# Kernel tuning notes

Hardware: AMD Instinct MI355X
Metric: run time of the kernel (lower is better)

The kernel has to match this reference:

```python
import jax, jax.numpy as jnp
import numpy as np

B, D_DATA, D_DICT0, N_SAE, D_DICT = 2048, 768, 128, 128, 32


def _kaiming_uniform(key, shape, fan_in):
    # torch.nn.init.kaiming_uniform_ default: bound = sqrt(6 / fan_in) / sqrt(5-gain stuff) ~ use gain=sqrt(2)? match torch default a=sqrt(5) not needed; plain kaiming_uniform_ uses gain=sqrt(2): bound = sqrt(6/fan_in)*? Keep simple: bound = sqrt(6.0/fan_in)
    bound = np.sqrt(6.0 / fan_in)
    return jax.random.uniform(key, shape, jnp.float32, -bound, bound)


def setup_inputs() -> dict:
    key = jax.random.key(0)
    ks = jax.random.split(key, 6)
    x = jax.random.normal(ks[0], (B, D_DATA), jnp.float32)
    # top-level SAE params
    W_enc0 = _kaiming_uniform(ks[1], (D_DATA, D_DICT0), D_DATA)
    b_enc0 = jnp.zeros((D_DICT0,), jnp.float32)
    W_dec0 = _kaiming_uniform(ks[2], (D_DICT0, D_DATA), D_DICT0)
    W_dec0 = W_dec0 / jnp.linalg.norm(W_dec0, axis=-1, keepdims=True)
    b_dec0 = jnp.zeros((D_DATA,), jnp.float32)
    # sublayer (hierarchical) per-expert params
    W_enc1 = _kaiming_uniform(ks[3], (N_SAE, D_DATA, D_DICT), D_DATA)
    b_enc1 = jnp.zeros((N_SAE, D_DICT), jnp.float32)
    W_dec1 = _kaiming_uniform(ks[4], (N_SAE, D_DICT, D_DATA), D_DICT)
    W_dec1 = W_dec1 / jnp.linalg.norm(W_dec1, axis=-1, keepdims=True)
    b_dec1 = jnp.zeros((N_SAE, D_DATA), jnp.float32)
    return {"x": x, "W_enc0": W_enc0, "b_enc0": b_enc0, "W_dec0": W_dec0,
            "b_dec0": b_dec0, "W_enc1": W_enc1, "b_enc1": b_enc1,
            "W_dec1": W_dec1, "b_dec1": b_dec1}


def reference(x, W_enc0, b_enc0, W_dec0, b_dec0, W_enc1, b_enc1, W_dec1, b_dec1):
    # ---- sae_0 (standard SAE; scale/unscale are identity) ----
    acts0 = jax.nn.relu((x - b_dec0) @ W_enc0 + b_enc0)        # [B, D_DICT0]
    x0 = acts0 @ W_dec0 + b_dec0                               # [B, D_DATA]
    # ---- binary gate over experts (n_sae == d_dict0) ----
    gate = (acts0 > 0).astype(x.dtype)                         # [B, N_SAE]
    # ---- sublayer: gather-encode-decode-scatter, expressed densely with a
    # binary mask (gate only selects membership; gate value is not multiplied).
    # Avoid materializing [B, N_SAE, D_DATA] by distributing (x - b_dec1[j]):
    pre = (jnp.einsum('bd,jdk->bjk', x, W_enc1)
           - jnp.einsum('jd,jdk->jk', b_dec1, W_enc1)[None]
           + b_enc1[None])                                     # [B, N_SAE, D_DICT]
    acts1 = jax.nn.relu(pre) * gate[:, :, None]                # zero out ungated
    # scatter_add over experts: sum_j gated (acts1[b,j] @ W_dec1[j] + b_dec1[j])
    dec = jnp.einsum('bjk,jkd->bd', acts1, W_dec1) + gate @ b_dec1  # [B, D_DATA]
    return x0 + dec
```

## Files before the change

kernel.cpp:

```cpp
#include <hip/hip_runtime.h>
#include <hip/hip_bf16.h>
#include <stdint.h>

#define B_SZ   2048
#define DDATA  768
#define NSAE   128
#define NJK    4096
#define KA2    4352
#define SPLITK 2
#define KC2    2176
#define GZCH   8
#define GZW    96

typedef unsigned short u16;
typedef short bf16x8 __attribute__((ext_vector_type(8)));
typedef float f32x4  __attribute__((ext_vector_type(4)));

static __device__ __forceinline__ u16 f2bf(float f) {
  __hip_bfloat16 h = __float2bfloat16(f);
  return *reinterpret_cast<u16*>(&h);
}

static __device__ __forceinline__ void gload16(const u16* g, u16* l) {
  __builtin_amdgcn_global_load_lds(
      (const __attribute__((address_space(1))) unsigned int*)g,
      (__attribute__((address_space(3))) unsigned int*)l,
      16, 0, 0);
}

__global__ __launch_bounds__(256) void k_front(const float* __restrict__ x,
                                               const float* __restrict__ We0,
                                               const float* __restrict__ bd0,
                                               const float* __restrict__ We1,
                                               const float* __restrict__ bd1,
                                               const float* __restrict__ be1,
                                               const float* __restrict__ Wd1,
                                               const float* __restrict__ Wd0,
                                               u16* __restrict__ W1T,
                                               float* __restrict__ cv,
                                               u16* __restrict__ B2T,
                                               u16* __restrict__ xb,
                                               float* __restrict__ pp,
                                               float* __restrict__ xnp,
                                               float* __restrict__ wn) {
  __shared__ float smem[64 * 65];
  const int bid = blockIdx.x, t = threadIdx.x;
  if (bid < 128) {
    const int j = bid;
    float* ts  = smem;
    float* bds = smem + 64 * 33;
    float* red = smem + 64 * 33 + 64;
    const int k = t & 31, g = t >> 5;
    float cacc = 0.f;
    for (int db = 0; db < 12; ++db) {
      const float* src = We1 + (size_t)j * 24576 + db * 2048;
#pragma unroll
      for (int i = 0; i < 8; ++i) {
        int e = t + i * 256;
        ts[(e >> 5) * 33 + (e & 31)] = src[e];
      }
      if (t < 64) bds[t] = bd1[(size_t)j * DDATA + db * 64 + t];
      __syncthreads();
#pragma unroll
      for (int i = 0; i < 8; ++i) {
        int e = t + i * 256;
        int kk = e >> 6, d = e & 63;
        W1T[(size_t)(j * 32 + kk) * DDATA + db * 64 + d] = f2bf(ts[d * 33 + kk]);
      }
#pragma unroll
      for (int q = 0; q < 8; ++q) {
        int d = g + 8 * q;
        cacc += ts[d * 33 + k] * bds[d];
      }
      __syncthreads();
    }
    red[g * 32 + k] = cacc;
    __syncthreads();
    if (g == 0) {
      float s = 0.f;
#pragma unroll
      for (int q = 0; q < 8; ++q) s += red[q * 32 + k];
      cv[j * 32 + k] = be1[j * 32 + k] - s;
    }
  } else if (bid < 944) {
    const int e2 = bid - 128;
    const int rb = e2 / 12, dbk = e2 % 12;
    const float* src; int r0, base;
    if (rb < 64)      { src = Wd1; r0 = rb * 64;        base = 0;    }
    else if (rb < 66) { src = Wd0; r0 = (rb - 64) * 64; base = 4096; }
    else              { src = bd1; r0 = (rb - 66) * 64; base = 4224; }
    const int d0 = dbk * 64;
#pragma unroll
    for (int i = 0; i < 16; ++i) {
      int e = t + i * 256;
      int ri = e >> 6, di = e & 63;
      smem[ri * 65 + di] = src[(size_t)(r0 + ri) * DDATA + d0 + di];
    }
    __syncthreads();
#pragma unroll
    for (int i = 0; i < 16; ++i) {
      int e = t + i * 256;
      int di = e >> 6, ri = e & 63;
      B2T[(size_t)(d0 + di) * KA2 + base + r0 + ri] = f2bf(smem[ri * 65 + di]);
    }
  } else if (bid < 952) {
    const int wb = bid - 944;
    const int jj = wb * 16 + (t >> 4), s = t & 15;
    float acc = 0.f;
    for (int d = s; d < DDATA; d += 16) {
      float w = We0[(size_t)d * 128 + jj];
      acc += w * w;
    }
#pragma unroll
    for (int sh = 8; sh; sh >>= 1) acc += __shfl_xor(acc, sh, 64);
    if (s == 0) wn[jj] = sqrtf(acc);
  } else {
    const int bid2 = bid - 952;
    const int b0 = (bid2 & 63) * 32, z = bid2 >> 6;
    const int dbase = z * GZW;
    float* xs = smem;
#pragma unroll
    for (int i = 0; i < 3; ++i) {
      int idx = t + i * 256;
      int r = idx / 24, c4 = idx % 24;
      size_t go = (size_t)(b0 + r) * DDATA + dbase + c4 * 4;
      float4 v = *(const float4*)&x[go];
      ushort4 o;
      o.x = f2bf(v.x); o.y = f2bf(v.y); o.z = f2bf(v.z); o.w = f2bf(v.w);
      *(ushort4*)&xb[go] = o;
      float4 b4 = *(const float4*)&bd0[dbase + c4 * 4];
      v.x -= b4.x; v.y -= b4.y; v.z -= b4.z; v.w -= b4.w;
      *(float4*)&xs[r * GZW + c4 * 4] = v;
    }
    __syncthreads();
    const int jp = t & 63, rg = t >> 6;
    const int j0 = jp * 2;
    float ap[8][2], xq[8];
#pragma unroll
    for (int r = 0; r < 8; ++r) { ap[r][0] = ap[r][1] = xq[r] = 0.f; }
    for (int d = 0; d < GZW; d += 4) {
      float4 xv[8];
#pragma unroll
      for (int r = 0; r < 8; ++r)
        xv[r] = *(const float4*)&xs[(rg * 8 + r) * GZW + d];
#pragma unroll
      for (int dd = 0; dd < 4; ++dd) {
        float2 w2 = *(const float2*)&We0[(size_t)(dbase + d + dd) * 128 + j0];
#pragma unroll
        for (int r = 0; r < 8; ++r) {
          float xr = ((const float*)&xv[r])[dd];
          ap[r][0] += xr * w2.x;
          ap[r][1] += xr * w2.y;
          xq[r]    += xr * xr;
        }
      }
    }
#pragma unroll
    for (int r = 0; r < 8; ++r) {
      size_t o = ((size_t)z * B_SZ + b0 + rg * 8 + r) * 128 + j0;
      *(float2*)&pp[o] = make_float2(ap[r][0], ap[r][1]);
    }
    if (jp == 0) {
#pragma unroll
      for (int r = 0; r < 8; ++r)
        xnp[(size_t)z * B_SZ + b0 + rg * 8 + r] = xq[r];
    }
  }
}

template<int BM, int BN, int EPI>
__global__ __launch_bounds__(256) void k_gemm(const u16* __restrict__ A,
                                              const u16* __restrict__ Bm,
                                              int K, int Kc,
                                              float* __restrict__ outF,
                                              u16* __restrict__ A2,
                                              const float* __restrict__ cvec,
                                              const float* __restrict__ pp,
                                              const float* __restrict__ xnp,
                                              const float* __restrict__ wnv,
                                              const float* __restrict__ be0,
                                              const float* __restrict__ x,
                                              const float* __restrict__ We0,
                                              const float* __restrict__ bd0) {
  constexpr int WM = BM / 32, WN = BN / 32;
  __shared__ __align__(16) u16 As[BM * 64];
  __shared__ __align__(16) u16 Bs[BN * 64];
  __shared__ u16 gate_s[BM * 4];
  __shared__ float cv_s[BN];
  const int tid = threadIdx.x;
  const int bx = blockIdx.x, by = blockIdx.y, bz = blockIdx.z;
  const int kbase = bz * Kc;
  const u16* Ab = A  + (size_t)(by * BM) * K;
  const u16* Bb = Bm + (size_t)(bx * BN) * K;
  const int wave = tid >> 6, lane = tid & 63;
  const int wr = wave >> 1, wc = wave & 1;
  const int m0 = wr * (BM / 2), n0 = wc * (BN / 2);
  const int lm = lane & 15, qd = lane >> 4;

  f32x4 acc[WM][WN];
  const f32x4 zero = {0.f, 0.f, 0.f, 0.f};
  for (int mi = 0; mi < WM; ++mi)
    for (int ni = 0; ni < WN; ++ni) acc[mi][ni] = zero;

  for (int k0 = kbase; k0 < kbase + Kc; k0 += 64) {
#pragma unroll
    for (int i = 0; i < BM / 32; ++i) {
      int id = tid + 256 * i;
      int row = id >> 3, u = id & 7;
      gload16(Ab + (size_t)row * K + k0 + ((u ^ (row & 7)) * 8), &As[id * 8]);
    }
#pragma unroll
    for (int i = 0; i < BN / 32; ++i) {
      int id = tid + 256 * i;
      int row = id >> 3, u = id & 7;
      gload16(Bb + (size_t)row * K + k0 + ((u ^ (row & 7)) * 8), &Bs[id * 8]);
    }
    __syncthreads();
#pragma unroll
    for (int s = 0; s < 2; ++s) {
      const int swz = ((s << 2) + qd) ^ (lm & 7);
      bf16x8 af[WM], bfv[WN];
#pragma unroll
      for (int mi = 0; mi < WM; ++mi)
        af[mi] = *(const bf16x8*)&As[(m0 + mi * 16 + lm) * 64 + swz * 8];
#pragma unroll
      for (int ni = 0; ni < WN; ++ni)
        bfv[ni] = *(const bf16x8*)&Bs[(n0 + ni * 16 + lm) * 64 + swz * 8];
#pragma unroll
      for (int mi = 0; mi < WM; ++mi)
#pragma unroll
        for (int ni = 0; ni < WN; ++ni)
          acc[mi][ni] = __builtin_amdgcn_mfma_f32_16x16x32_bf16(af[mi], bfv[ni],
                                                                acc[mi][ni], 0, 0, 0);
    }
    __syncthreads();
  }

  if (EPI == 1) {
#pragma unroll
    for (int e0 = 0; e0 < BM * 4; e0 += 256) {
      int e = e0 + tid;
      int r = e >> 2, q = e & 3;
      int gb = by * BM + r, gj = bx * 4 + q;
      float p = be0[gj], xn2 = 0.f;
#pragma unroll
      for (int z = 0; z < GZCH; ++z) {
        p   += pp[((size_t)z * B_SZ + gb) * 128 + gj];
        xn2 += xnp[(size_t)z * B_SZ + gb];
      }
      float tau = 1e-4f * sqrtf(xn2) * wnv[gj];
      unsigned long long mask = __ballot(fabsf(p) <= tau);
      while (mask) {
        int src = (int)__builtin_ctzll(mask);
        mask &= mask - 1;
        int bb = __shfl(gb, src, 64), jj = __shfl(gj, src, 64);
        double dacc = 0.0;
#pragma unroll
        for (int tt = 0; tt < 12; ++tt) {
          int d = lane + tt * 64;
          dacc += (double)(x[(size_t)bb * DDATA + d] - bd0[d]) *
                  (double)We0[(size_t)d * 128 + jj];
        }
#pragma unroll
        for (int s = 32; s; s >>= 1) dacc += __shfl_xor(dacc, s, 64);
        double pd = dacc + (double)be0[jj];
        if (lane == src) p = (float)pd;
      }
      u16 gbit = (p > 0.f) ? (u16)0x3F80 : (u16)0;
      gate_s[e] = gbit;
      size_t row = (size_t)gb * KA2;
      A2[row + NJK + gj]       = f2bf(p > 0.f ? p : 0.f);
      A2[row + NJK + 128 + gj] = gbit;
    }
    for (int e = tid; e < BN; e += 256) cv_s[e] = cvec[bx * BN + e];
    __syncthreads();
  }

  const int rb = qd * 4;
#pragma unroll
  for (int mi = 0; mi < WM; ++mi) {
#pragma unroll
    for (int ni = 0; ni < WN; ++ni) {
#pragma unroll
      for (int r = 0; r < 4; ++r) {
        int ml = m0 + mi * 16 + rb + r;
        int nl = n0 + ni * 16 + lm;
        int gm = by * BM + ml;
        int gn = bx * BN + nl;
        float v = acc[mi][ni][r];
        if (EPI == 1) {
          v += cv_s[nl];
          v = v > 0.f ? v : 0.f;
          u16 gbit = gate_s[ml * 4 + (nl >> 5)];
          v = gbit ? v : 0.f;
          float vn = __shfl_xor(v, 1, 64);
          if ((lm & 1) == 0) {
            unsigned pk = (unsigned)f2bf(v) | ((unsigned)f2bf(vn) << 16);
            *(unsigned*)&A2[(size_t)gm * KA2 + gn] = pk;
          }
        } else {
          outF[((size_t)bz * B_SZ + gm) * DDATA + gn] = v;
        }
      }
    }
  }
}

__global__ __launch_bounds__(256) void k_reduce(const float* __restrict__ part,
                                                const float* __restrict__ bias,
                                                float* __restrict__ out) {
  const int N4 = B_SZ * DDATA / 4;
  int i = blockIdx.x * 256 + threadIdx.x;
  const float4* p4 = (const float4*)part;
  float4 s = p4[i];
#pragma unroll
  for (int z = 1; z < SPLITK; ++z) {
    float4 t = p4[i + z * N4];
    s.x += t.x; s.y += t.y; s.z += t.z; s.w += t.w;
  }
  float4 b = ((const float4*)bias)[i % (DDATA / 4)];
  s.x += b.x; s.y += b.y; s.z += b.z; s.w += b.w;
  ((float4*)out)[i] = s;
}

extern "C" void kernel_launch(void* const* d_in, const int* in_sizes, int n_in,
                              void* d_out, int out_size, void* d_ws, size_t ws_size,
                              hipStream_t stream) {
  const float* x   = (const float*)d_in[0];
  const float* We0 = (const float*)d_in[1];
  const float* be0 = (const float*)d_in[2];
  const float* Wd0 = (const float*)d_in[3];
  const float* bd0 = (const float*)d_in[4];
  const float* We1 = (const float*)d_in[5];
  const float* be1 = (const float*)d_in[6];
  const float* Wd1 = (const float*)d_in[7];
  const float* bd1 = (const float*)d_in[8];
  float* out = (float*)d_out;

  uint8_t* ws = (uint8_t*)d_ws;
  size_t off = 0;
  auto carve = [&](size_t bytes) {
    uint8_t* p = ws + off;
    off += (bytes + 255) & ~(size_t)255;
    return p;
  };
  u16*    A2   = (u16*)carve((size_t)B_SZ * KA2 * 2);
  u16*    xb   = (u16*)carve((size_t)B_SZ * DDATA * 2);
  u16*    W1T  = (u16*)carve((size_t)NJK * DDATA * 2);
  u16*    B2T  = (u16*)carve((size_t)DDATA * KA2 * 2);
  float*  cv   = (float*)carve((size_t)NJK * 4);
  float*  part = (float*)carve((size_t)SPLITK * B_SZ * DDATA * 4);
  float*  pp   = (float*)carve((size_t)GZCH * B_SZ * 128 * 4);
  float*  xnp  = (float*)carve((size_t)GZCH * B_SZ * 4);
  float*  wn   = (float*)carve(128 * 4);

  k_front <<<1464, 256, 0, stream>>>(x, We0, bd0, We1, bd1, be1, Wd1, Wd0,
                                     W1T, cv, B2T, xb, pp, xnp, wn);
  k_gemm<128, 128, 1><<<dim3(32, 16, 1), 256, 0, stream>>>(
      xb, W1T, DDATA, DDATA, nullptr, A2, cv, pp, xnp, wn, be0, x, We0, bd0);
  k_gemm<64, 128, 2><<<dim3(6, 32, SPLITK), 256, 0, stream>>>(
      A2, B2T, KA2, KC2, part, nullptr, nullptr,
      nullptr, nullptr, nullptr, nullptr, nullptr, nullptr, nullptr);
  k_reduce<<<1536, 256, 0, stream>>>(part, bd0, out);
}
```

Before: 186.3 us.

## Compute sae_0 gate fully in front kernel and shrink second GEMM tile

Moves the whole sae_0 encoder (full-D reduction, column norms, threshold refinement, acts0 and gate writes into A2) into 64 blocks of the front kernel, removing the split-D partial buffers and the epilogue reduction from the first GEMM. The first GEMM now only loads gate bits and cv before its main loop. The second GEMM tile changes from 64x128 to 32x128, doubling its grid. The trade-off is that the 64 front blocks become long serial chains covering all 768 dimensions, which can leave them as stragglers in the front kernel and reduce parallelism there.

Result: slower. 222.1 us (+19.2%).

```diff
diff --git a/kernel.cpp b/kernel.cpp
--- a/kernel.cpp
+++ b/kernel.cpp
@@ -9,7 +9,6 @@
 #define KA2    4352
 #define SPLITK 2
 #define KC2    2176
-#define GZCH   8
 #define GZW    96
 
 typedef unsigned short u16;
@@ -30,6 +29,7 @@
 
 __global__ __launch_bounds__(256) void k_front(const float* __restrict__ x,
                                                const float* __restrict__ We0,
+                                               const float* __restrict__ be0,
                                                const float* __restrict__ bd0,
                                                const float* __restrict__ We1,
                                                const float* __restrict__ bd1,
@@ -40,13 +40,89 @@
                                                float* __restrict__ cv,
                                                u16* __restrict__ B2T,
                                                u16* __restrict__ xb,
-                                               float* __restrict__ pp,
-                                               float* __restrict__ xnp,
-                                               float* __restrict__ wn) {
+                                               u16* __restrict__ A2) {
   __shared__ float smem[64 * 65];
   const int bid = blockIdx.x, t = threadIdx.x;
-  if (bid < 128) {
-    const int j = bid;
+  if (bid < 64) {
+    const int b0 = bid * 32;
+    float* xs = smem;
+    const int jp = t & 63, rg = t >> 6;
+    const int lane = t & 63;
+    const int j0 = jp * 2;
+    float ap[8][2], xq[8], wq[2];
+#pragma unroll
+    for (int r = 0; r < 8; ++r) { ap[r][0] = ap[r][1] = xq[r] = 0.f; }
+    wq[0] = wq[1] = 0.f;
+    for (int z = 0; z < 8; ++z) {
+      const int dbase = z * GZW;
+#pragma unroll
+      for (int i = 0; i < 3; ++i) {
+        int idx = t + i * 256;
+        int r = idx / 24, c4 = idx % 24;
+        size_t go = (size_t)(b0 + r) * DDATA + dbase + c4 * 4;
+        float4 v = *(const float4*)&x[go];
+        ushort4 o;
+        o.x = f2bf(v.x); o.y = f2bf(v.y); o.z = f2bf(v.z); o.w = f2bf(v.w);
+        *(ushort4*)&xb[go] = o;
+        float4 b4 = *(const float4*)&bd0[dbase + c4 * 4];
+        v.x -= b4.x; v.y -= b4.y; v.z -= b4.z; v.w -= b4.w;
+        *(float4*)&xs[r * GZW + c4 * 4] = v;
+      }
+      __syncthreads();
+      for (int d = 0; d < GZW; d += 4) {
+        float4 xv[8];
+#pragma unroll
+        for (int r = 0; r < 8; ++r)
+          xv[r] = *(const float4*)&xs[(rg * 8 + r) * GZW + d];
+#pragma unroll
+        for (int dd = 0; dd < 4; ++dd) {
+          float2 w2 = *(const float2*)&We0[(size_t)(dbase + d + dd) * 128 + j0];
+          wq[0] += w2.x * w2.x;
+          wq[1] += w2.y * w2.y;
+#pragma unroll
+          for (int r = 0; r < 8; ++r) {
+            float xr = ((const float*)&xv[r])[dd];
+            ap[r][0] += xr * w2.x;
+            ap[r][1] += xr * w2.y;
+            xq[r]    += xr * xr;
+          }
+        }
+      }
+      __syncthreads();
+    }
+    const float be0v0 = be0[j0], be0v1 = be0[j0 + 1];
+    const float wn0 = sqrtf(wq[0]), wn1 = sqrtf(wq[1]);
+#pragma unroll
+    for (int r = 0; r < 8; ++r) {
+#pragma unroll
+      for (int c = 0; c < 2; ++c) {
+        int gb = b0 + rg * 8 + r, gj = j0 + c;
+        float p = (c ? be0v1 : be0v0) + ap[r][c];
+        float tau = 1e-4f * sqrtf(xq[r]) * (c ? wn1 : wn0);
+        unsigned long long mask = __ballot(fabsf(p) <= tau);
+        while (mask) {
+          int src = (int)__builtin_ctzll(mask);
+          mask &= mask - 1;
+          int bb = __shfl(gb, src, 64), jj = __shfl(gj, src, 64);
+          double dacc = 0.0;
+#pragma unroll
+          for (int tt = 0; tt < 12; ++tt) {
+            int d = lane + tt * 64;
+            dacc += (double)(x[(size_t)bb * DDATA + d] - bd0[d]) *
+                    (double)We0[(size_t)d * 128 + jj];
+          }
+#pragma unroll
+          for (int s = 32; s; s >>= 1) dacc += __shfl_xor(dacc, s, 64);
+          double pd = dacc + (double)be0[jj];
+          if (lane == src) p = (float)pd;
+        }
+        size_t row = (size_t)gb * KA2;
+        A2[row + NJK + gj]       = f2bf(p > 0.f ? p : 0.f);
+        A2[row + NJK + 128 + gj] = (p > 0.f) ? (u16)0x3F80 : (u16)0;
+      }
+    }
+  } else if (bid < 192) {
+    const int j = bid - 64;
     float* ts  = smem;
     float* bds = smem + 64 * 33;
     float* red = smem + 64 * 33 + 64;
@@ -82,8 +158,8 @@
       for (int q = 0; q < 8; ++q) s += red[q * 32 + k];
       cv[j * 32 + k] = be1[j * 32 + k] - s;
     }
-  } else if (bid < 944) {
-    const int e2 = bid - 128;
+  } else {
+    const int e2 = bid - 192;
     const int rb = e2 / 12, dbk = e2 % 12;
     const float* src; int r0, base;
     if (rb < 64)      { src = Wd1; r0 = rb * 64;        base = 0;    }
@@ -103,68 +179,6 @@
       int di = e >> 6, ri = e & 63;
       B2T[(size_t)(d0 + di) * KA2 + base + r0 + ri] = f2bf(smem[ri * 65 + di]);
     }
-  } else if (bid < 952) {
-    const int wb = bid - 944;
-    const int jj = wb * 16 + (t >> 4), s = t & 15;
-    float acc = 0.f;
-    for (int d = s; d < DDATA; d += 16) {
-      float w = We0[(size_t)d * 128 + jj];
-      acc += w * w;
-    }
-#pragma unroll
-    for (int sh = 8; sh; sh >>= 1) acc += __shfl_xor(acc, sh, 64);
-    if (s == 0) wn[jj] = sqrtf(acc);
-  } else {
-    const int bid2 = bid - 952;
-    const int b0 = (bid2 & 63) * 32, z = bid2 >> 6;
-    const int dbase = z * GZW;
-    float* xs = smem;
-#pragma unroll
-    for (int i = 0; i < 3; ++i) {
-      int idx = t + i * 256;
-      int r = idx / 24, c4 = idx % 24;
-      size_t go = (size_t)(b0 + r) * DDATA + dbase + c4 * 4;
-      float4 v = *(const float4*)&x[go];
-      ushort4 o;
-      o.x = f2bf(v.x); o.y = f2bf(v.y); o.z = f2bf(v.z); o.w = f2bf(v.w);
-      *(ushort4*)&xb[go] = o;
-      float4 b4 = *(const float4*)&bd0[dbase + c4 * 4];
-      v.x -= b4.x; v.y -= b4.y; v.z -= b4.z; v.w -= b4.w;
-      *(float4*)&xs[r * GZW + c4 * 4] = v;
-    }
-    __syncthreads();
-    const int jp = t & 63, rg = t >> 6;
-    const int j0 = jp * 2;
-    float ap[8][2], xq[8];
-#pragma unroll
-    for (int r = 0; r < 8; ++r) { ap[r][0] = ap[r][1] = xq[r] = 0.f; }
-    for (int d = 0; d < GZW; d += 4) {
-      float4 xv[8];
-#pragma unroll
-      for (int r = 0; r < 8; ++r)
-        xv[r] = *(const float4*)&xs[(rg * 8 + r) * GZW + d];
-#pragma unroll
-      for (int dd = 0; dd < 4; ++dd) {
-        float2 w2 = *(const float2*)&We0[(size_t)(dbase + d + dd) * 128 + j0];
-#pragma unroll
-        for (int r = 0; r < 8; ++r) {
-          float xr = ((const float*)&xv[r])[dd];
-          ap[r][0] += xr * w2.x;
-          ap[r][1] += xr * w2.y;
-          xq[r]    += xr * xr;
-        }
-      }
-    }
-#pragma unroll
-    for (int r = 0; r < 8; ++r) {
-      size_t o = ((size_t)z * B_SZ + b0 + rg * 8 + r) * 128 + j0;
-      *(float2*)&pp[o] = make_float2(ap[r][0], ap[r][1]);
-    }
-    if (jp == 0) {
-#pragma unroll
-      for (int r = 0; r < 8; ++r)
-        xnp[(size_t)z * B_SZ + b0 + rg * 8 + r] = xq[r];
-    }
   }
 }
 
@@ -174,14 +188,7 @@
                                               int K, int Kc,
                                               float* __restrict__ outF,
                                               u16* __restrict__ A2,
-                                              const float* __restrict__ cvec,
-                                              const float* __restrict__ pp,
-                                              const float* __restrict__ xnp,
-                                              const float* __restrict__ wnv,
-                                              const float* __restrict__ be0,
-                                              const float* __restrict__ x,
-                                              const float* __restrict__ We0,
-                                              const float* __restrict__ bd0) {
+                                              const float* __restrict__ cvec) {
   constexpr int WM = BM / 32, WN = BN / 32;
   __shared__ __align__(16) u16 As[BM * 64];
   __shared__ __align__(16) u16 Bs[BN * 64];
@@ -197,6 +204,14 @@
   const int m0 = wr * (BM / 2), n0 = wc * (BN / 2);
   const int lm = lane & 15, qd = lane >> 4;
 
+  if (EPI == 1) {
+    for (int e = tid; e < BM * 4; e += 256) {
+      int r = e >> 2, q = e & 3;
+      gate_s[e] = A2[(size_t)(by * BM + r) * KA2 + NJK + 128 + bx * 4 + q];
+    }
+    for (int e = tid; e < BN; e += 256) cv_s[e] = cvec[bx * BN + e];
+  }
+
   f32x4 acc[WM][WN];
   const f32x4 zero = {0.f, 0.f, 0.f, 0.f};
   for (int mi = 0; mi < WM; ++mi)
@@ -233,46 +248,6 @@
           acc[mi][ni] = __builtin_amdgcn_mfma_f32_16x16x32_bf16(af[mi], bfv[ni],
                                                                 acc[mi][ni], 0, 0, 0);
     }
-    __syncthreads();
-  }
-
-  if (EPI == 1) {
-#pragma unroll
-    for (int e0 = 0; e0 < BM * 4; e0 += 256) {
-      int e = e0 + tid;
-      int r = e >> 2, q = e & 3;
-      int gb = by * BM + r, gj = bx * 4 + q;
-      float p = be0[gj], xn2 = 0.f;
-#pragma unroll
-      for (int z = 0; z < GZCH; ++z) {
-        p   += pp[((size_t)z * B_SZ + gb) * 128 + gj];
-        xn2 += xnp[(size_t)z * B_SZ + gb];
-      }
-      float tau = 1e-4f * sqrtf(xn2) * wnv[gj];
-      unsigned long long mask = __ballot(fabsf(p) <= tau);
-      while (mask) {
-        int src = (int)__builtin_ctzll(mask);
-        mask &= mask - 1;
-        int bb = __shfl(gb, src, 64), jj = __shfl(gj, src, 64);
-        double dacc = 0.0;
-#pragma unroll
-        for (int tt = 0; tt < 12; ++tt) {
-          int d = lane + tt * 64;
-          dacc += (double)(x[(size_t)bb * DDATA + d] - bd0[d]) *
-                  (double)We0[(size_t)d * 128 + jj];
-        }
-#pragma unroll
-        for (int s = 32; s; s >>= 1) dacc += __shfl_xor(dacc, s, 64);
-        double pd = dacc + (double)be0[jj];
-        if (lane == src) p = (float)pd;
-      }
-      u16 gbit = (p > 0.f) ? (u16)0x3F80 : (u16)0;
-      gate_s[e] = gbit;
-      size_t row = (size_t)gb * KA2;
-      A2[row + NJK + gj]       = f2bf(p > 0.f ? p : 0.f);
-      A2[row + NJK + 128 + gj] = gbit;
-    }
-    for (int e = tid; e < BN; e += 256) cv_s[e] = cvec[bx * BN + e];
     __syncthreads();
   }
 
@@ -350,16 +325,12 @@
   u16*    B2T  = (u16*)carve((size_t)DDATA * KA2 * 2);
   float*  cv   = (float*)carve((size_t)NJK * 4);
   float*  part = (float*)carve((size_t)SPLITK * B_SZ * DDATA * 4);
-  float*  pp   = (float*)carve((size_t)GZCH * B_SZ * 128 * 4);
-  float*  xnp  = (float*)carve((size_t)GZCH * B_SZ * 4);
-  float*  wn   = (float*)carve(128 * 4);
-
-  k_front <<<1464, 256, 0, stream>>>(x, We0, bd0, We1, bd1, be1, Wd1, Wd0,
-                                     W1T, cv, B2T, xb, pp, xnp, wn);
-  k_gemm<128, 128, 1><<<dim3(32, 16, 1), 256, 0, stream>>>(
-      xb, W1T, DDATA, DDATA, nullptr, A2, cv, pp, xnp, wn, be0, x, We0, bd0);
-  k_gemm<64, 128, 2><<<dim3(6, 32, SPLITK), 256, 0, stream>>>(
-      A2, B2T, KA2, KC2, part, nullptr, nullptr,
-      nullptr, nullptr, nullptr, nullptr, nullptr, nullptr, nullptr);
+
+  k_front <<<1008, 256, 0, stream>>>(x, We0, be0, bd0, We1, bd1, be1, Wd1, Wd0,
+                                     W1T, cv, B2T, xb, A2);
+  k_gemm<128, 128, 1><<<dim3(32, 16, 1), 256, 0, stream>>>(xb, W1T, DDATA, DDATA,
+                                                           nullptr, A2, cv);
+  k_gemm<32, 128, 2><<<dim3(6, 64, SPLITK), 256, 0, stream>>>(A2, B2T, KA2, KC2,
+                                                              part, nullptr, nullptr);
   k_reduce<<<1536, 256, 0, stream>>>(part, bd0, out);
 }
```
